# Kernel tuning notes

Hardware: AMD Instinct MI355X
Metric: run time of the kernel (lower is better)

The kernel has to match this reference:

```python
import jax, jax.numpy as jnp
import numpy as np

B, T, D = 2, 2048, 1024
N, H = 16, 64  # num_heads, head_dim


def setup_inputs() -> dict:
    key = jax.random.key(0)
    ks = jax.random.split(key, 8)
    glorot = lambda k, shape, fan_in, fan_out: jax.random.uniform(
        k, shape, jnp.float32, -1.0, 1.0) * np.sqrt(6.0 / (fan_in + fan_out))
    return {
        "q": jax.random.normal(ks[0], (B, T, D), jnp.float32),
        "v": jax.random.normal(ks[1], (B, T, D), jnp.float32),
        "k": jax.random.normal(ks[2], (B, T, D), jnp.float32),
        "w_query": glorot(ks[3], (D, N, H), D, N * H),
        "b_query": jnp.zeros((N, 1, H), jnp.float32),
        "w_value": glorot(ks[4], (D, N, H), D, N * H),
        "b_value": jnp.zeros((N, 1, H), jnp.float32),
        "w_key": glorot(ks[5], (D, N, H), D, N * H),
        "b_key": jnp.zeros((N, 1, H), jnp.float32),
        "w_projection": glorot(ks[6], (N, D, H), N * H, D),
        "b_projection": jnp.zeros((1, D), jnp.float32),
    }


def reference(q, v, k, w_query, b_query, w_value, b_value, w_key, b_key,
              w_projection, b_projection):
    # QKV projections: [B,T,D] x [D,N,H] -> [B,N,T,H]
    query = jnp.einsum('btd,dnh->bnth', q, w_query) + b_query
    value = jnp.einsum('btd,dnh->bnth', v, w_value) + b_value
    key_p = jnp.einsum('btd,dnh->bnth', k, w_key) + b_key
    # Scaled dot-product attention, scores divided by sqrt(head_dim)
    scale = 1.0 / jnp.sqrt(jnp.asarray(H, query.dtype))
    scores = jnp.einsum('bnth,bnsh->bnts', query, key_p) * scale  # [B,N,T,T]
    weights = jax.nn.softmax(scores, axis=-1)
    attn = jnp.einsum('bnts,bnsh->bnth', weights, value)
    # Output projection: [B,N,T,H] x [N,D,H] -> [B,T,D]
    out = jnp.einsum('bnth,ndh->btd', attn, w_projection) + b_projection
    return out
```

## Files before the change

### kernel.cpp

```cpp
#include <hip/hip_runtime.h>
#include <hip/hip_bf16.h>
#include <cstdint>
#include <cstddef>


typedef __attribute__((ext_vector_type(8))) short short8;
typedef __attribute__((ext_vector_type(4))) float floatx4;
typedef __attribute__((ext_vector_type(8))) unsigned short ushort8;

#define EXP2F(x) __builtin_amdgcn_exp2f(x)

static __device__ __forceinline__ unsigned short f2bf(float f) {
    union { float f; unsigned int u; } v; v.f = f;
    unsigned int r = v.u + 0x7fffu + ((v.u >> 16) & 1u);
    return (unsigned short)(r >> 16);
}
static __device__ __forceinline__ unsigned int pk2bf(float lo, float hi) {
    __hip_bfloat162 t = __float22bfloat162_rn(make_float2(lo, hi));
    union { __hip_bfloat162 h; unsigned int u; } c; c.h = t;
    return c.u;
}
static __device__ __forceinline__ void gl_lds16(const unsigned short* g, unsigned short* l) {
    __builtin_amdgcn_global_load_lds(
        (const __attribute__((address_space(1))) unsigned int*)g,
        (__attribute__((address_space(3))) unsigned int*)l, 16, 0, 0);
}

__global__ __launch_bounds__(256) void mha_transpose_w(
    const float* __restrict__ wq, const float* __restrict__ wk, const float* __restrict__ wv,
    unsigned short* __restrict__ wqT, unsigned short* __restrict__ wkT, unsigned short* __restrict__ wvT)
{
    __shared__ float tile[32][33];
    const float* src; unsigned short* dst;
    int z = blockIdx.z;
    if (z == 0)      { src = wq; dst = wqT; }
    else if (z == 1) { src = wk; dst = wkT; }
    else             { src = wv; dst = wvT; }
    int n0 = blockIdx.x * 32, d0 = blockIdx.y * 32;
    int tx = threadIdx.x, ty = threadIdx.y;
    #pragma unroll
    for (int j = 0; j < 4; ++j)
        tile[ty + j * 8][tx] = src[(size_t)(d0 + ty + j * 8) * 1024 + n0 + tx];
    __syncthreads();
    #pragma unroll
    for (int j = 0; j < 4; ++j)
        dst[(size_t)(n0 + ty + j * 8) * 1024 + d0 + tx] = f2bf(tile[tx][ty + j * 8]);
}

__global__ __launch_bounds__(256) void mha_reorder_wp(
    const float* __restrict__ wp, unsigned short* __restrict__ wp2)
{
    int base = blockIdx.x * 1024 + threadIdx.x;
    #pragma unroll
    for (int i = 0; i < 4; ++i) {
        int idx = base + i * 256;
        int n = idx >> 16, d = (idx >> 6) & 1023, h = idx & 63;
        wp2[(size_t)d * 1024 + n * 64 + h] = f2bf(wp[idx]);
    }
}

__global__ __launch_bounds__(256) void mha_tr_v(
    const unsigned short* __restrict__ Vp, unsigned short* __restrict__ Vt)
{
    __shared__ unsigned short tile[64][72];
    int bn = blockIdx.x, tb = blockIdx.y;
    int tid = threadIdx.x;
    const unsigned short* src = Vp + ((size_t)bn * 2048 + tb * 64) * 64;
    unsigned short* dst = Vt + (size_t)bn * 64 * 2048 + tb * 64;
    int r = tid >> 2, cq = (tid & 3) * 16;
    *(ushort8*)&tile[r][cq]     = *(const ushort8*)(src + r * 64 + cq);
    *(ushort8*)&tile[r][cq + 8] = *(const ushort8*)(src + r * 64 + cq + 8);
    __syncthreads();
    int h = tid >> 2, t0 = (tid & 3) * 16;
    ushort8 o0, o1;
    #pragma unroll
    for (int j = 0; j < 8; ++j) { o0[j] = tile[t0 + j][h]; o1[j] = tile[t0 + 8 + j][h]; }
    *(ushort8*)(dst + (size_t)h * 2048 + t0)     = o0;
    *(ushort8*)(dst + (size_t)h * 2048 + t0 + 8) = o1;
}

__global__ __launch_bounds__(256) void gemm_qkv128(
    const float* __restrict__ A0, const float* __restrict__ A1, const float* __restrict__ A2,
    const unsigned short* __restrict__ W0, const unsigned short* __restrict__ W1,
    const unsigned short* __restrict__ W2,
    const float* __restrict__ b0, const float* __restrict__ b1, const float* __restrict__ b2,
    unsigned short* __restrict__ O0, unsigned short* __restrict__ O1, unsigned short* __restrict__ O2,
    float qscale)
{
    __shared__ unsigned short As[128 * 32];
    __shared__ unsigned short Bs[128 * 32];
    int bm = blockIdx.x, by = blockIdx.y;
    int mat = by >> 3, nt = by & 7;
    const float* A           = mat == 0 ? A0 : (mat == 1 ? A1 : A2);
    const unsigned short* WT = mat == 0 ? W0 : (mat == 1 ? W1 : W2);
    const float* bias        = mat == 0 ? b0 : (mat == 1 ? b1 : b2);
    unsigned short* Out      = mat == 0 ? O0 : (mat == 1 ? O1 : O2);
    float scale = (mat == 0) ? qscale : 1.0f;

    int tid = threadIdx.x;
    int w = tid >> 6, lane = tid & 63, c15 = lane & 15, quad = lane >> 4;
    int wm = w >> 1, wn = w & 1;

    const float* gAf[2]; unsigned short* lA[2];
    const unsigned short* gB[2]; unsigned short* lB[2];
    #pragma unroll
    for (int i = 0; i < 2; ++i) {
        int s = (w * 2 + i) * 64 + lane;
        gAf[i] = A + (size_t)(bm * 128 + (s >> 2)) * 1024 + (s & 3) * 8;
        lA[i] = &As[s * 8];
        gB[i] = WT + (size_t)(nt * 128 + (s >> 2)) * 1024 + (s & 3) * 8;
        lB[i] = &Bs[s * 8];
    }

    floatx4 acc[4][4];
    #pragma unroll
    for (int mi = 0; mi < 4; ++mi)
        #pragma unroll
        for (int ni = 0; ni < 4; ++ni) acc[mi][ni] = (floatx4){0.f, 0.f, 0.f, 0.f};

    float4 af4[2][2];
    #pragma unroll
    for (int i = 0; i < 2; ++i) {
        af4[i][0] = *(const float4*)(gAf[i]);
        af4[i][1] = *(const float4*)(gAf[i] + 4);
    }

    for (int kt = 0; kt < 32; ++kt) {
        __syncthreads();
        #pragma unroll
        for (int i = 0; i < 2; ++i) {
            gl_lds16(gB[i] + kt * 32, lB[i]);
            uint4 pk;
            pk.x = pk2bf(af4[i][0].x, af4[i][0].y);
            pk.y = pk2bf(af4[i][0].z, af4[i][0].w);
            pk.z = pk2bf(af4[i][1].x, af4[i][1].y);
            pk.w = pk2bf(af4[i][1].z, af4[i][1].w);
            *(uint4*)lA[i] = pk;
        }
        if (kt < 31) {
            #pragma unroll
            for (int i = 0; i < 2; ++i) {
                af4[i][0] = *(const float4*)(gAf[i] + (kt + 1) * 32);
                af4[i][1] = *(const float4*)(gAf[i] + (kt + 1) * 32 + 4);
            }
        }
        __syncthreads();
        short8 af[4], bfr[4];
        #pragma unroll
        for (int mi = 0; mi < 4; ++mi)
            af[mi] = *(const short8*)&As[(wm * 64 + mi * 16 + c15) * 32 + quad * 8];
        #pragma unroll
        for (int ni = 0; ni < 4; ++ni)
            bfr[ni] = *(const short8*)&Bs[(wn * 64 + ni * 16 + c15) * 32 + quad * 8];
        #pragma unroll
        for (int mi = 0; mi < 4; ++mi)
            #pragma unroll
            for (int ni = 0; ni < 4; ++ni)
                acc[mi][ni] = __builtin_amdgcn_mfma_f32_16x16x32_bf16(af[mi], bfr[ni], acc[mi][ni], 0, 0, 0);
    }
    #pragma unroll
    for (int mi = 0; mi < 4; ++mi)
        #pragma unroll
        for (int ni = 0; ni < 4; ++ni)
            #pragma unroll
            for (int r = 0; r < 4; ++r) {
                int row = bm * 128 + wm * 64 + mi * 16 + quad * 4 + r;
                int col = nt * 128 + wn * 64 + ni * 16 + c15;
                float val = (acc[mi][ni][r] + bias[col]) * scale;
                int b = row >> 11, t = row & 2047, n = col >> 6, h = col & 63;
                Out[((size_t)(b * 16 + n) * 2048 + t) * 64 + h] = f2bf(val);
            }
}

__global__ __launch_bounds__(256) void mha_flash3(
    const unsigned short* __restrict__ Qp, const unsigned short* __restrict__ Kp,
    const unsigned short* __restrict__ Vt, unsigned short* __restrict__ attnb)
{
    __shared__ unsigned short Ks[64 * 72];
    __shared__ unsigned short Vs[64 * 72];
    __shared__ unsigned short Pl[4][32 * 72];

    int bi = blockIdx.x;
    int xcd = bi & 7, j = bi >> 3;
    int bn = xcd * 4 + (j >> 4), qt = j & 15;
    int b = bn >> 4, n = bn & 15;
    int tid = threadIdx.x;
    int w = tid >> 6, lane = tid & 63, c15 = lane & 15, quad = lane >> 4;

    const unsigned short* Qb = Qp + (size_t)bn * 2048 * 64;
    const unsigned short* Kb = Kp + (size_t)bn * 2048 * 64;
    const unsigned short* Vb = Vt + (size_t)bn * 64 * 2048;

    int qbase = qt * 128 + w * 32;

    short8 bQ[2][2];
    #pragma unroll
    for (int tni = 0; tni < 2; ++tni)
        #pragma unroll
        for (int kc = 0; kc < 2; ++kc)
            bQ[tni][kc] = *(const short8*)(Qb + (size_t)(qbase + tni * 16 + c15) * 64 + kc * 32 + quad * 8);

    float l_i[2] = {0.f, 0.f};
    floatx4 o[2][4];
    #pragma unroll
    for (int i = 0; i < 2; ++i)
        #pragma unroll
        for (int j2 = 0; j2 < 4; ++j2) o[i][j2] = (floatx4){0.f, 0.f, 0.f, 0.f};

    unsigned short* Pw = &Pl[w][0];
    int srow = tid >> 3, scc = tid & 7;

    ushort8 kreg[2], vreg[2];
    #pragma unroll
    for (int i = 0; i < 2; ++i) {
        kreg[i] = *(const ushort8*)(Kb + (size_t)(srow + i * 32) * 64 + scc * 8);
        vreg[i] = *(const ushort8*)(Vb + (size_t)(srow + i * 32) * 2048 + scc * 8);
    }

    for (int it = 0; it < 32; ++it) {
        __syncthreads();
        #pragma unroll
        for (int i = 0; i < 2; ++i) {
            *(ushort8*)&Ks[(srow + i * 32) * 72 + scc * 8] = kreg[i];
            *(ushort8*)&Vs[(srow + i * 32) * 72 + scc * 8] = vreg[i];
        }
        if (it < 31) {
            int s1 = (it + 1) * 64;
            #pragma unroll
            for (int i = 0; i < 2; ++i) {
                kreg[i] = *(const ushort8*)(Kb + (size_t)(s1 + srow + i * 32) * 64 + scc * 8);
                vreg[i] = *(const ushort8*)(Vb + (size_t)(srow + i * 32) * 2048 + s1 + scc * 8);
            }
        }
        __syncthreads();

        floatx4 sc[4][2];
        #pragma unroll
        for (int smi = 0; smi < 4; ++smi) {
            short8 a0 = *(const short8*)&Ks[(smi * 16 + c15) * 72 + quad * 8];
            short8 a1 = *(const short8*)&Ks[(smi * 16 + c15) * 72 + 32 + quad * 8];
            #pragma unroll
            for (int tni = 0; tni < 2; ++tni) {
                floatx4 t = (floatx4){0.f, 0.f, 0.f, 0.f};
                t = __builtin_amdgcn_mfma_f32_16x16x32_bf16(a0, bQ[tni][0], t, 0, 0, 0);
                t = __builtin_amdgcn_mfma_f32_16x16x32_bf16(a1, bQ[tni][1], t, 0, 0, 0);
                sc[smi][tni] = t;
            }
        }
        #pragma unroll
        for (int tni = 0; tni < 2; ++tni) {
            float rs = 0.f;
            #pragma unroll
            for (int smi = 0; smi < 4; ++smi) {
                float p0 = EXP2F(sc[smi][tni][0]);
                float p1 = EXP2F(sc[smi][tni][1]);
                float p2 = EXP2F(sc[smi][tni][2]);
                float p3 = EXP2F(sc[smi][tni][3]);
                rs += (p0 + p1) + (p2 + p3);
                uint2 pw;
                pw.x = pk2bf(p0, p1);
                pw.y = pk2bf(p2, p3);
                *(uint2*)&Pw[(tni * 16 + c15) * 72 + smi * 16 + quad * 4] = pw;
            }
            l_i[tni] += rs;
        }
        short8 bv[4][2];
        #pragma unroll
        for (int hni = 0; hni < 4; ++hni)
            #pragma unroll
            for (int kc = 0; kc < 2; ++kc)
                bv[hni][kc] = *(const short8*)&Vs[(hni * 16 + c15) * 72 + kc * 32 + quad * 8];
        #pragma unroll
        for (int tmi = 0; tmi < 2; ++tmi) {
            short8 ap0 = *(const short8*)&Pw[(tmi * 16 + c15) * 72 + quad * 8];
            short8 ap1 = *(const short8*)&Pw[(tmi * 16 + c15) * 72 + 32 + quad * 8];
            #pragma unroll
            for (int hni = 0; hni < 4; ++hni) {
                o[tmi][hni] = __builtin_amdgcn_mfma_f32_16x16x32_bf16(ap0, bv[hni][0], o[tmi][hni], 0, 0, 0);
                o[tmi][hni] = __builtin_amdgcn_mfma_f32_16x16x32_bf16(ap1, bv[hni][1], o[tmi][hni], 0, 0, 0);
            }
        }
    }
    float lf[2];
    #pragma unroll
    for (int tmi = 0; tmi < 2; ++tmi) {
        float s = l_i[tmi];
        s += __shfl_xor(s, 16, 64);
        s += __shfl_xor(s, 32, 64);
        lf[tmi] = s;
    }
    #pragma unroll
    for (int tmi = 0; tmi < 2; ++tmi)
        #pragma unroll
        for (int r = 0; r < 4; ++r) {
            float linv = 1.0f / __shfl(lf[tmi], quad * 4 + r, 64);
            int t = qbase + tmi * 16 + quad * 4 + r;
            #pragma unroll
            for (int hni = 0; hni < 4; ++hni) {
                int col = n * 64 + hni * 16 + c15;
                attnb[(size_t)(b * 2048 + t) * 1024 + col] = f2bf(o[tmi][hni][r] * linv);
            }
        }
}

__global__ __launch_bounds__(256) void gemm_out64v2(
    const unsigned short* __restrict__ A, const unsigned short* __restrict__ BT,
    const float* __restrict__ bias, float* __restrict__ out)
{
    __shared__ unsigned short As[64 * 64];
    __shared__ unsigned short Bs[128 * 64];
    int g = blockIdx.x + (blockIdx.y << 6);
    int nt = g & 7, bm = g >> 3;
    int tid = threadIdx.x;
    int w = tid >> 6, lane = tid & 63, c15 = lane & 15, quad = lane >> 4;
    int wm = w >> 1, wn = w & 1;

    const unsigned short* gA[2]; unsigned short* lA[2];
    const unsigned short* gB[4]; unsigned short* lB[4];
    #pragma unroll
    for (int i = 0; i < 2; ++i) {
        int s = (w * 2 + i) * 64 + lane;
        int row = s >> 3, cl = (s & 7) ^ (row & 7);
        gA[i] = A + (size_t)(bm * 64 + row) * 1024 + cl * 8;
        lA[i] = &As[s * 8];
    }
    #pragma unroll
    for (int i = 0; i < 4; ++i) {
        int s = (w * 4 + i) * 64 + lane;
        int row = s >> 3, cl = (s & 7) ^ (row & 7);
        gB[i] = BT + (size_t)(nt * 128 + row) * 1024 + cl * 8;
        lB[i] = &Bs[s * 8];
    }

    floatx4 acc[2][4];
    #pragma unroll
    for (int mi = 0; mi < 2; ++mi)
        #pragma unroll
        for (int ni = 0; ni < 4; ++ni) acc[mi][ni] = (floatx4){0.f, 0.f, 0.f, 0.f};

    for (int kt = 0; kt < 16; ++kt) {
        __syncthreads();
        #pragma unroll
        for (int i = 0; i < 2; ++i) gl_lds16(gA[i] + kt * 64, lA[i]);
        #pragma unroll
        for (int i = 0; i < 4; ++i) gl_lds16(gB[i] + kt * 64, lB[i]);
        __syncthreads();
        #pragma unroll
        for (int kc = 0; kc < 2; ++kc) {
            short8 af[2], bfr[4];
            #pragma unroll
            for (int mi = 0; mi < 2; ++mi) {
                int row = wm * 32 + mi * 16 + c15;
                af[mi] = *(const short8*)&As[row * 64 + (((kc * 4 + quad) ^ (row & 7)) * 8)];
            }
            #pragma unroll
            for (int ni = 0; ni < 4; ++ni) {
                int row = wn * 64 + ni * 16 + c15;
                bfr[ni] = *(const short8*)&Bs[row * 64 + (((kc * 4 + quad) ^ (row & 7)) * 8)];
            }
            #pragma unroll
            for (int mi = 0; mi < 2; ++mi)
                #pragma unroll
                for (int ni = 0; ni < 4; ++ni)
                    acc[mi][ni] = __builtin_amdgcn_mfma_f32_16x16x32_bf16(af[mi], bfr[ni], acc[mi][ni], 0, 0, 0);
        }
    }
    #pragma unroll
    for (int mi = 0; mi < 2; ++mi)
        #pragma unroll
        for (int ni = 0; ni < 4; ++ni)
            #pragma unroll
            for (int r = 0; r < 4; ++r) {
                int row = bm * 64 + wm * 32 + mi * 16 + quad * 4 + r;
                int col = nt * 128 + wn * 64 + ni * 16 + c15;
                out[(size_t)row * 1024 + col] = acc[mi][ni][r] + bias[col];
            }
}

extern "C" void kernel_launch(void* const* d_in, const int* in_sizes, int n_in,
                              void* d_out, int out_size, void* d_ws, size_t ws_size,
                              hipStream_t stream)
{
    const float* q  = (const float*)d_in[0];
    const float* v  = (const float*)d_in[1];
    const float* k  = (const float*)d_in[2];
    const float* wq = (const float*)d_in[3];
    const float* bq = (const float*)d_in[4];
    const float* wv = (const float*)d_in[5];
    const float* bv = (const float*)d_in[6];
    const float* wk = (const float*)d_in[7];
    const float* bk = (const float*)d_in[8];
    const float* wp = (const float*)d_in[9];
    const float* bp = (const float*)d_in[10];
    float* out = (float*)d_out;

    char* ws = (char*)d_ws;
    unsigned short* wqT  = (unsigned short*)(ws + (size_t)0);
    unsigned short* wkT  = (unsigned short*)(ws + ((size_t)2  << 20));
    unsigned short* wvT  = (unsigned short*)(ws + ((size_t)4  << 20));
    unsigned short* wp2  = (unsigned short*)(ws + ((size_t)6  << 20));
    unsigned short* Qp   = (unsigned short*)(ws + ((size_t)8  << 20));
    unsigned short* Kp   = (unsigned short*)(ws + ((size_t)16 << 20));
    unsigned short* Vtp  = (unsigned short*)(ws + ((size_t)24 << 20));
    unsigned short* Vp   = (unsigned short*)(ws + ((size_t)32 << 20));
    unsigned short* attnb= (unsigned short*)(ws + ((size_t)32 << 20));

    const float qscale = 0.125f * 1.44269504088896f;

    hipLaunchKernelGGL(mha_transpose_w, dim3(32, 32, 3), dim3(32, 8), 0, stream,
                       wq, wk, wv, wqT, wkT, wvT);
    hipLaunchKernelGGL(mha_reorder_wp, dim3(1024), dim3(256), 0, stream, wp, wp2);

    hipLaunchKernelGGL(gemm_qkv128, dim3(32, 24), dim3(256), 0, stream,
                       q, k, v, wqT, wkT, wvT, bq, bk, bv, Qp, Kp, Vp, qscale);
    hipLaunchKernelGGL(mha_tr_v, dim3(32, 32), dim3(256), 0, stream, Vp, Vtp);

    hipLaunchKernelGGL(mha_flash3, dim3(512), dim3(256), 0, stream, Qp, Kp, Vtp, attnb);
    hipLaunchKernelGGL(gemm_out64v2, dim3(64, 8), dim3(256), 0, stream, attnb, wp2, bp, out);
}
```

Before: 234.5 us.

## Fuse weight prep kernels, write V transposed from QKV GEMM, async-load fp32 A

Merges the QKV weight transpose and output-weight reorder into one launch. The QKV GEMM now writes V directly in transposed layout, which removes the separate V transpose kernel and its round trip through memory. The fp32 activation tile is now streamed into a swizzled LDS buffer with global_load_lds and converted to bf16 when the fragments are read, replacing the register prefetch. In flash attention, the second barrier moves ahead of the next K/V prefetch. The transposed V stores are strided and uncoalesced, and the fp32 LDS tile doubles the A-tile shared memory.

```diff
diff --git a/kernel.cpp b/kernel.cpp
--- a/kernel.cpp
+++ b/kernel.cpp
@@ -25,58 +25,43 @@
         (const __attribute__((address_space(1))) unsigned int*)g,
         (__attribute__((address_space(3))) unsigned int*)l, 16, 0, 0);
 }
-
-__global__ __launch_bounds__(256) void mha_transpose_w(
+static __device__ __forceinline__ void gl_lds16f(const float* g, float* l) {
+    __builtin_amdgcn_global_load_lds(
+        (const __attribute__((address_space(1))) unsigned int*)g,
+        (__attribute__((address_space(3))) unsigned int*)l, 16, 0, 0);
+}
+
+__global__ __launch_bounds__(256) void mha_prep_w(
     const float* __restrict__ wq, const float* __restrict__ wk, const float* __restrict__ wv,
-    unsigned short* __restrict__ wqT, unsigned short* __restrict__ wkT, unsigned short* __restrict__ wvT)
+    const float* __restrict__ wp,
+    unsigned short* __restrict__ wqT, unsigned short* __restrict__ wkT,
+    unsigned short* __restrict__ wvT, unsigned short* __restrict__ wp2)
 {
     __shared__ float tile[32][33];
-    const float* src; unsigned short* dst;
     int z = blockIdx.z;
-    if (z == 0)      { src = wq; dst = wqT; }
-    else if (z == 1) { src = wk; dst = wkT; }
-    else             { src = wv; dst = wvT; }
-    int n0 = blockIdx.x * 32, d0 = blockIdx.y * 32;
-    int tx = threadIdx.x, ty = threadIdx.y;
-    #pragma unroll
-    for (int j = 0; j < 4; ++j)
-        tile[ty + j * 8][tx] = src[(size_t)(d0 + ty + j * 8) * 1024 + n0 + tx];
-    __syncthreads();
-    #pragma unroll
-    for (int j = 0; j < 4; ++j)
-        dst[(size_t)(n0 + ty + j * 8) * 1024 + d0 + tx] = f2bf(tile[tx][ty + j * 8]);
-}
-
-__global__ __launch_bounds__(256) void mha_reorder_wp(
-    const float* __restrict__ wp, unsigned short* __restrict__ wp2)
-{
-    int base = blockIdx.x * 1024 + threadIdx.x;
-    #pragma unroll
-    for (int i = 0; i < 4; ++i) {
-        int idx = base + i * 256;
-        int n = idx >> 16, d = (idx >> 6) & 1023, h = idx & 63;
-        wp2[(size_t)d * 1024 + n * 64 + h] = f2bf(wp[idx]);
-    }
-}
-
-__global__ __launch_bounds__(256) void mha_tr_v(
-    const unsigned short* __restrict__ Vp, unsigned short* __restrict__ Vt)
-{
-    __shared__ unsigned short tile[64][72];
-    int bn = blockIdx.x, tb = blockIdx.y;
     int tid = threadIdx.x;
-    const unsigned short* src = Vp + ((size_t)bn * 2048 + tb * 64) * 64;
-    unsigned short* dst = Vt + (size_t)bn * 64 * 2048 + tb * 64;
-    int r = tid >> 2, cq = (tid & 3) * 16;
-    *(ushort8*)&tile[r][cq]     = *(const ushort8*)(src + r * 64 + cq);
-    *(ushort8*)&tile[r][cq + 8] = *(const ushort8*)(src + r * 64 + cq + 8);
-    __syncthreads();
-    int h = tid >> 2, t0 = (tid & 3) * 16;
-    ushort8 o0, o1;
-    #pragma unroll
-    for (int j = 0; j < 8; ++j) { o0[j] = tile[t0 + j][h]; o1[j] = tile[t0 + 8 + j][h]; }
-    *(ushort8*)(dst + (size_t)h * 2048 + t0)     = o0;
-    *(ushort8*)(dst + (size_t)h * 2048 + t0 + 8) = o1;
+    if (z < 3) {
+        const float* src = z == 0 ? wq : (z == 1 ? wk : wv);
+        unsigned short* dst = z == 0 ? wqT : (z == 1 ? wkT : wvT);
+        int n0 = blockIdx.x * 32, d0 = blockIdx.y * 32;
+        int tx = tid & 31, ty = tid >> 5;
+        #pragma unroll
+        for (int j = 0; j < 4; ++j)
+            tile[ty + j * 8][tx] = src[(size_t)(d0 + ty + j * 8) * 1024 + n0 + tx];
+        __syncthreads();
+        #pragma unroll
+        for (int j = 0; j < 4; ++j)
+            dst[(size_t)(n0 + ty + j * 8) * 1024 + d0 + tx] = f2bf(tile[tx][ty + j * 8]);
+    } else {
+        int bid = blockIdx.x + blockIdx.y * 32;
+        int base = bid * 1024 + tid;
+        #pragma unroll
+        for (int i = 0; i < 4; ++i) {
+            int idx = base + i * 256;
+            int n = idx >> 16, d = (idx >> 6) & 1023, h = idx & 63;
+            wp2[(size_t)d * 1024 + n * 64 + h] = f2bf(wp[idx]);
+        }
+    }
 }
 
 __global__ __launch_bounds__(256) void gemm_qkv128(
@@ -87,7 +72,7 @@
     unsigned short* __restrict__ O0, unsigned short* __restrict__ O1, unsigned short* __restrict__ O2,
     float qscale)
 {
-    __shared__ unsigned short As[128 * 32];
+    __shared__ float Asf[128 * 32];
     __shared__ unsigned short Bs[128 * 32];
     int bm = blockIdx.x, by = blockIdx.y;
     int mat = by >> 3, nt = by & 7;
@@ -96,18 +81,24 @@
     const float* bias        = mat == 0 ? b0 : (mat == 1 ? b1 : b2);
     unsigned short* Out      = mat == 0 ? O0 : (mat == 1 ? O1 : O2);
     float scale = (mat == 0) ? qscale : 1.0f;
+    int vmode = (mat == 2);
 
     int tid = threadIdx.x;
     int w = tid >> 6, lane = tid & 63, c15 = lane & 15, quad = lane >> 4;
     int wm = w >> 1, wn = w & 1;
 
-    const float* gAf[2]; unsigned short* lA[2];
+    const float* gA[4]; float* lA[4];
+    #pragma unroll
+    for (int i = 0; i < 4; ++i) {
+        int s = (w * 4 + i) * 64 + lane;
+        int row = s >> 3, cl4 = (s & 7) ^ ((row & 3) << 1);
+        gA[i] = A + (size_t)(bm * 128 + row) * 1024 + cl4 * 4;
+        lA[i] = &Asf[s * 4];
+    }
     const unsigned short* gB[2]; unsigned short* lB[2];
     #pragma unroll
     for (int i = 0; i < 2; ++i) {
         int s = (w * 2 + i) * 64 + lane;
-        gAf[i] = A + (size_t)(bm * 128 + (s >> 2)) * 1024 + (s & 3) * 8;
-        lA[i] = &As[s * 8];
         gB[i] = WT + (size_t)(nt * 128 + (s >> 2)) * 1024 + (s & 3) * 8;
         lB[i] = &Bs[s * 8];
     }
@@ -118,37 +109,25 @@
         #pragma unroll
         for (int ni = 0; ni < 4; ++ni) acc[mi][ni] = (floatx4){0.f, 0.f, 0.f, 0.f};
 
-    float4 af4[2][2];
-    #pragma unroll
-    for (int i = 0; i < 2; ++i) {
-        af4[i][0] = *(const float4*)(gAf[i]);
-        af4[i][1] = *(const float4*)(gAf[i] + 4);
-    }
-
     for (int kt = 0; kt < 32; ++kt) {
         __syncthreads();
         #pragma unroll
-        for (int i = 0; i < 2; ++i) {
-            gl_lds16(gB[i] + kt * 32, lB[i]);
-            uint4 pk;
-            pk.x = pk2bf(af4[i][0].x, af4[i][0].y);
-            pk.y = pk2bf(af4[i][0].z, af4[i][0].w);
-            pk.z = pk2bf(af4[i][1].x, af4[i][1].y);
-            pk.w = pk2bf(af4[i][1].z, af4[i][1].w);
-            *(uint4*)lA[i] = pk;
-        }
-        if (kt < 31) {
-            #pragma unroll
-            for (int i = 0; i < 2; ++i) {
-                af4[i][0] = *(const float4*)(gAf[i] + (kt + 1) * 32);
-                af4[i][1] = *(const float4*)(gAf[i] + (kt + 1) * 32 + 4);
-            }
-        }
+        for (int i = 0; i < 4; ++i) gl_lds16f(gA[i] + kt * 32, lA[i]);
+        #pragma unroll
+        for (int i = 0; i < 2; ++i) gl_lds16(gB[i] + kt * 32, lB[i]);
         __syncthreads();
         short8 af[4], bfr[4];
         #pragma unroll
-        for (int mi = 0; mi < 4; ++mi)
-            af[mi] = *(const short8*)&As[(wm * 64 + mi * 16 + c15) * 32 + quad * 8];
+        for (int mi = 0; mi < 4; ++mi) {
+            int row = wm * 64 + mi * 16 + c15;
+            int oc = (quad ^ (row & 3)) * 8;
+            float4 a0 = *(const float4*)&Asf[row * 32 + oc];
+            float4 a1 = *(const float4*)&Asf[row * 32 + oc + 4];
+            union { uint4 u; short8 s; } cv;
+            cv.u.x = pk2bf(a0.x, a0.y); cv.u.y = pk2bf(a0.z, a0.w);
+            cv.u.z = pk2bf(a1.x, a1.y); cv.u.w = pk2bf(a1.z, a1.w);
+            af[mi] = cv.s;
+        }
         #pragma unroll
         for (int ni = 0; ni < 4; ++ni)
             bfr[ni] = *(const short8*)&Bs[(wn * 64 + ni * 16 + c15) * 32 + quad * 8];
@@ -168,7 +147,10 @@
                 int col = nt * 128 + wn * 64 + ni * 16 + c15;
                 float val = (acc[mi][ni][r] + bias[col]) * scale;
                 int b = row >> 11, t = row & 2047, n = col >> 6, h = col & 63;
-                Out[((size_t)(b * 16 + n) * 2048 + t) * 64 + h] = f2bf(val);
+                if (vmode)
+                    Out[((size_t)(b * 16 + n) * 64 + h) * 2048 + t] = f2bf(val);
+                else
+                    Out[((size_t)(b * 16 + n) * 2048 + t) * 64 + h] = f2bf(val);
             }
 }
 
@@ -224,6 +206,7 @@
             *(ushort8*)&Ks[(srow + i * 32) * 72 + scc * 8] = kreg[i];
             *(ushort8*)&Vs[(srow + i * 32) * 72 + scc * 8] = vreg[i];
         }
+        __syncthreads();
         if (it < 31) {
             int s1 = (it + 1) * 64;
             #pragma unroll
@@ -232,7 +215,6 @@
                 vreg[i] = *(const ushort8*)(Vb + (size_t)(srow + i * 32) * 2048 + s1 + scc * 8);
             }
         }
-        __syncthreads();
 
         floatx4 sc[4][2];
         #pragma unroll
@@ -402,19 +384,14 @@
     unsigned short* Qp   = (unsigned short*)(ws + ((size_t)8  << 20));
     unsigned short* Kp   = (unsigned short*)(ws + ((size_t)16 << 20));
     unsigned short* Vtp  = (unsigned short*)(ws + ((size_t)24 << 20));
-    unsigned short* Vp   = (unsigned short*)(ws + ((size_t)32 << 20));
     unsigned short* attnb= (unsigned short*)(ws + ((size_t)32 << 20));
 
     const float qscale = 0.125f * 1.44269504088896f;
 
-    hipLaunchKernelGGL(mha_transpose_w, dim3(32, 32, 3), dim3(32, 8), 0, stream,
-                       wq, wk, wv, wqT, wkT, wvT);
-    hipLaunchKernelGGL(mha_reorder_wp, dim3(1024), dim3(256), 0, stream, wp, wp2);
-
+    hipLaunchKernelGGL(mha_prep_w, dim3(32, 32, 4), dim3(256), 0, stream,
+                       wq, wk, wv, wp, wqT, wkT, wvT, wp2);
     hipLaunchKernelGGL(gemm_qkv128, dim3(32, 24), dim3(256), 0, stream,
-                       q, k, v, wqT, wkT, wvT, bq, bk, bv, Qp, Kp, Vp, qscale);
-    hipLaunchKernelGGL(mha_tr_v, dim3(32, 32), dim3(256), 0, stream, Vp, Vtp);
-
+                       q, k, v, wqT, wkT, wvT, bq, bk, bv, Qp, Kp, Vtp, qscale);
     hipLaunchKernelGGL(mha_flash3, dim3(512), dim3(256), 0, stream, Qp, Kp, Vtp, attnb);
     hipLaunchKernelGGL(gemm_out64v2, dim3(64, 8), dim3(256), 0, stream, attnb, wp2, bp, out);
 }
```

Result: no change. 233.5 us (-0.4%).
